# Kernel tuning notes

Measured on AMD Instinct MI355X. Metric: run time of the kernel, lower is better.

Reference implementation:

```python
import jax, jax.numpy as jnp
import numpy as np

NUM_EXPERTS = 8
TOP_K = 2
HIDDEN = 1024
INTER = 3584
TOKENS = 16384


def setup_inputs() -> dict:
    key = jax.random.key(0)
    k0, k1, k2, k3, k4 = jax.random.split(key, 5)
    s = 0.02
    return {
        "hidden_states": jax.random.normal(k0, (TOKENS, HIDDEN), dtype=jnp.float32),
        "gate_w": jax.random.normal(k1, (NUM_EXPERTS, HIDDEN), dtype=jnp.float32) * s,
        "w1": jax.random.normal(k2, (NUM_EXPERTS, INTER, HIDDEN), dtype=jnp.float32) * s,
        "w3": jax.random.normal(k3, (NUM_EXPERTS, INTER, HIDDEN), dtype=jnp.float32) * s,
        "w2": jax.random.normal(k4, (NUM_EXPERTS, HIDDEN, INTER), dtype=jnp.float32) * s,
    }


def reference(hidden_states, gate_w, w1, w3, w2):
    # Router: logits -> softmax -> top-k -> renormalize (Mixtral gating)
    router_logits = jnp.einsum("th,eh->te", hidden_states, gate_w)  # [T, E]
    probs = jax.nn.softmax(router_logits, axis=-1)
    topk_w, topk_idx = jax.lax.top_k(probs, TOP_K)                  # [T, K]
    topk_w = topk_w / jnp.sum(topk_w, axis=-1, keepdims=True)
    # Dense combine weights: [T, E], zero for unselected experts
    combine = jnp.sum(
        jax.nn.one_hot(topk_idx, NUM_EXPERTS, dtype=hidden_states.dtype)
        * topk_w[..., None],
        axis=1,
    )
    out = jnp.zeros_like(hidden_states)
    for e in range(NUM_EXPERTS):  # small fixed expert loop
        h = jnp.einsum("th,ih->ti", hidden_states, w1[e])   # gate proj
        u = jnp.einsum("th,ih->ti", hidden_states, w3[e])   # up proj
        act = jax.nn.silu(h) * u                             # SwiGLU
        y = jnp.einsum("ti,hi->th", act, w2[e])              # down proj
        out = out + combine[:, e:e + 1] * y
    return out
```

## Files before the change

### kernel.cpp

```cpp
#include <hip/hip_runtime.h>
#include <hip/hip_bf16.h>

#define T_TOKENS 16384
#define HID 1024
#define NEXP 8
#define INTER 3584
#define PAIRS (2*T_TOKENS)
#define PAD_MAX (PAIRS + NEXP*128)

using f32x4    = __attribute__((ext_vector_type(4))) float;
using bfrag    = __attribute__((ext_vector_type(8))) short;
using float4_t = __attribute__((ext_vector_type(4))) float;
using ushort8_t = __attribute__((ext_vector_type(8))) unsigned short;

__device__ inline unsigned short f2bf(float f){
    unsigned u = __float_as_uint(f);
    u += 0x7FFFu + ((u >> 16) & 1u);
    return (unsigned short)(u >> 16);
}

__device__ inline void gload16(const unsigned short* g, unsigned short* l){
    __builtin_amdgcn_global_load_lds(
        (const __attribute__((address_space(1))) void*)g,
        (__attribute__((address_space(3))) void*)l, 16, 0, 0);
}

#define BAR_VM8() asm volatile("s_waitcnt vmcnt(8)\n\ts_barrier" ::: "memory")
#define BAR_VM0() asm volatile("s_waitcnt vmcnt(0)\n\ts_barrier" ::: "memory")
#define BAR_PLAIN() asm volatile("s_barrier" ::: "memory")

__device__ inline int xcd_swz(int flat, int nwg){
    int q = nwg >> 3, r = nwg & 7;
    int xcd = flat & 7, idx = flat >> 3;
    return (xcd < r ? xcd*(q+1) : r*(q+1) + (xcd - r)*q) + idx;
}

__device__ inline void st_decode(int sw, int nM, int nP, int STM,
                                 int& mt, int& p){
    int stSize = STM * nP;
    int st = sw / stSize;
    int rem = sw - st * stSize;
    int base = st * STM;
    int stM = (base + STM <= nM) ? STM : (nM - base);
    p  = rem / stM;
    mt = base + (rem - p * stM);
}

__global__ __launch_bounds__(256) void conv3_kernel(
    const float* __restrict__ w1, const float* __restrict__ w3,
    const float* __restrict__ w2,
    unsigned short* __restrict__ w1b, unsigned short* __restrict__ w3b,
    unsigned short* __restrict__ w2b)
{
    const int n = NEXP * INTER * HID;
    const float* in = (blockIdx.y == 0) ? w1 : (blockIdx.y == 1) ? w3 : w2;
    unsigned short* out = (blockIdx.y == 0) ? w1b : (blockIdx.y == 1) ? w3b : w2b;
    int i0 = (blockIdx.x * 256 + threadIdx.x) * 8;
    int stride = gridDim.x * 256 * 8;
    for (int i = i0; i < n; i += stride){
        float4_t a = *reinterpret_cast<const float4_t*>(in + i);
        float4_t b = *reinterpret_cast<const float4_t*>(in + i + 4);
        ushort8_t o;
        o[0]=f2bf(a.x); o[1]=f2bf(a.y); o[2]=f2bf(a.z); o[3]=f2bf(a.w);
        o[4]=f2bf(b.x); o[5]=f2bf(b.y); o[6]=f2bf(b.z); o[7]=f2bf(b.w);
        *reinterpret_cast<ushort8_t*>(out + i) = o;
    }
}

__global__ __launch_bounds__(256) void router_kernel(
    const float* __restrict__ x, const float* __restrict__ gw,
    int* __restrict__ topk_idx, float* __restrict__ topk_w,
    unsigned short* __restrict__ xb)
{
    int wave = threadIdx.x >> 6;
    int lane = threadIdx.x & 63;
    int t = blockIdx.x * 4 + wave;

    float acc[NEXP];
#pragma unroll
    for (int e = 0; e < NEXP; ++e) acc[e] = 0.f;

    const float* xr = x + (size_t)t * HID;
    for (int hb = 0; hb < HID; hb += 64){
        float xv = xr[hb + lane];
#pragma unroll
        for (int e = 0; e < NEXP; ++e)
            acc[e] += xv * gw[e * HID + hb + lane];
    }

    unsigned short* xbr = xb + (size_t)t * HID;
#pragma unroll
    for (int r = 0; r < 2; ++r){
        int c = (lane + r*64) * 8;
        float4_t va = *reinterpret_cast<const float4_t*>(xr + c);
        float4_t vb = *reinterpret_cast<const float4_t*>(xr + c + 4);
        ushort8_t o;
        o[0]=f2bf(va.x); o[1]=f2bf(va.y); o[2]=f2bf(va.z); o[3]=f2bf(va.w);
        o[4]=f2bf(vb.x); o[5]=f2bf(vb.y); o[6]=f2bf(vb.z); o[7]=f2bf(vb.w);
        *reinterpret_cast<ushort8_t*>(xbr + c) = o;
    }

#pragma unroll
    for (int e = 0; e < NEXP; ++e){
#pragma unroll
        for (int s = 32; s > 0; s >>= 1)
            acc[e] += __shfl_xor(acc[e], s, 64);
    }
    if (lane == 0){
        int e0 = 0; float m0 = acc[0];
#pragma unroll
        for (int e = 1; e < NEXP; ++e) if (acc[e] > m0){ m0 = acc[e]; e0 = e; }
        int e1 = -1; float m1 = -1e30f;
#pragma unroll
        for (int e = 0; e < NEXP; ++e) if (e != e0 && acc[e] > m1){ m1 = acc[e]; e1 = e; }
        float p1 = __expf(m1 - m0);
        float inv = 1.f / (1.f + p1);
        topk_idx[2*t]   = e0;
        topk_idx[2*t+1] = e1;
        topk_w[2*t]   = inv;
        topk_w[2*t+1] = p1 * inv;
    }
}

__global__ __launch_bounds__(256) void hist_kernel(
    const int* __restrict__ topk_idx, int* __restrict__ counts)
{
    __shared__ int h[NEXP];
    if (threadIdx.x < NEXP) h[threadIdx.x] = 0;
    __syncthreads();
    int i0 = blockIdx.x * 256 + threadIdx.x;
    for (int i = i0; i < PAIRS; i += gridDim.x * 256)
        atomicAdd(&h[topk_idx[i]], 1);
    __syncthreads();
    if (threadIdx.x < NEXP) atomicAdd(&counts[threadIdx.x], h[threadIdx.x]);
}

__global__ void scan_kernel(const int* __restrict__ counts, int* __restrict__ offp)
{
    if (threadIdx.x == 0 && blockIdx.x == 0){
        int s = 0;
        for (int e = 0; e < NEXP; ++e){
            offp[e] = s;
            s += (counts[e] + 127) & ~127;
        }
        offp[NEXP] = s;
    }
}

__global__ __launch_bounds__(128) void padfill_kernel(
    const int* __restrict__ counts, const int* __restrict__ offp,
    int* __restrict__ pair_token, float* __restrict__ pair_w)
{
    int e = blockIdx.x;
    int base = offp[e];
    int aligned = offp[e+1] - base;
    for (int s = counts[e] + threadIdx.x; s < aligned; s += 128){
        pair_token[base + s] = (base + s) & (T_TOKENS - 1);
        pair_w[base + s] = 0.f;
    }
}

__global__ __launch_bounds__(256) void scatter_kernel(
    const int* __restrict__ topk_idx, const float* __restrict__ topk_w,
    const int* __restrict__ offp, int* __restrict__ cursors,
    int* __restrict__ pair_token, float* __restrict__ pair_w)
{
    __shared__ int hist[NEXP], base[NEXP], lcur[NEXP];
    int tid = threadIdx.x;
    if (tid < NEXP){ hist[tid] = 0; lcur[tid] = 0; }
    __syncthreads();

    int t = blockIdx.x * 256 + tid;
    int e0 = topk_idx[2*t], e1 = topk_idx[2*t + 1];
    atomicAdd(&hist[e0], 1);
    atomicAdd(&hist[e1], 1);
    __syncthreads();

    if (tid < NEXP) base[tid] = atomicAdd(&cursors[tid], hist[tid]);
    __syncthreads();

    int r0 = atomicAdd(&lcur[e0], 1);
    int r1 = atomicAdd(&lcur[e1], 1);
    int p0 = offp[e0] + base[e0] + r0;
    int p1 = offp[e1] + base[e1] + r1;
    pair_token[p0] = t;  pair_w[p0] = topk_w[2*t];
    pair_token[p1] = t;  pair_w[p1] = topk_w[2*t + 1];
}

__global__ __launch_bounds__(256) void gemm_act_kernel(
    const unsigned short* __restrict__ xb,
    const unsigned short* __restrict__ w1b,
    const unsigned short* __restrict__ w3b,
    const int* __restrict__ offp,
    const int* __restrict__ pair_token, const float* __restrict__ pair_w,
    unsigned short* __restrict__ act, int r0)
{
    int nP = gridDim.x, nM = gridDim.y;
    int sw = xcd_swz(blockIdx.y * nP + blockIdx.x, nP * nM);
    int mt, p;
    st_decode(sw, nM, nP, 8, mt, p);
    int by = mt, bx = p;

    int R = r0 + by * 128;
    if (R >= offp[NEXP]) return;
    int e = 0;
    while (offp[e+1] <= R) ++e;
    int icol0 = bx * 64;

    __shared__ alignas(16) unsigned short As0[128*64], As1[128*64];
    __shared__ alignas(16) unsigned short B10[64*64],  B11[64*64];
    __shared__ alignas(16) unsigned short B30[64*64],  B31[64*64];
    __shared__ int   toks[128];
    __shared__ float pws[128];

    int tid = threadIdx.x;
    if (tid < 128){
        toks[tid] = pair_token[R + tid];
        pws[tid]  = pair_w[R + tid];
    }
    __syncthreads();

    int w = tid >> 6, lane = tid & 63;
    int wm = w >> 1, wn = w & 1;
    int lr = lane >> 3;
    int l15 = lane & 15;
    int swz8 = ((lane & 7) ^ lr) * 8;

    size_t asrc[4];
#pragma unroll
    for (int i = 0; i < 4; ++i)
        asrc[i] = (size_t)toks[w*32 + i*8 + lr] * HID + swz8;

    const unsigned short* w1e = w1b + (size_t)e * INTER * HID;
    const unsigned short* w3e = w3b + (size_t)e * INTER * HID;
    size_t bsrc[2];
#pragma unroll
    for (int i = 0; i < 2; ++i)
        bsrc[i] = (size_t)(icol0 + w*16 + i*8 + lr) * HID + swz8;

    int ccol[2];
#pragma unroll
    for (int kk = 0; kk < 2; ++kk)
        ccol[kk] = (((kk*4 + (lane >> 4)) ^ (lane & 7)) * 8);

    f32x4 acc_h[4][2], acc_u[4][2];
#pragma unroll
    for (int m = 0; m < 4; ++m)
#pragma unroll
        for (int n = 0; n < 2; ++n){
            acc_h[m][n] = (f32x4){0.f,0.f,0.f,0.f};
            acc_u[m][n] = (f32x4){0.f,0.f,0.f,0.f};
        }

    auto stageT = [&](unsigned short* As, unsigned short* B1s, unsigned short* B3s, int t){
        int k0 = t * 64;
#pragma unroll
        for (int i = 0; i < 4; ++i) gload16(xb  + asrc[i] + k0, As  + (w*32 + i*8)*64);
#pragma unroll
        for (int i = 0; i < 2; ++i) gload16(w1e + bsrc[i] + k0, B1s + (w*16 + i*8)*64);
#pragma unroll
        for (int i = 0; i < 2; ++i) gload16(w3e + bsrc[i] + k0, B3s + (w*16 + i*8)*64);
    };

    auto computeT = [&](const unsigned short* As, const unsigned short* B1s, const unsigned short* B3s){
        __builtin_amdgcn_s_setprio(1);
#pragma unroll
        for (int kk = 0; kk < 2; ++kk){
            int cc = ccol[kk];
            bfrag a[4];
#pragma unroll
            for (int m = 0; m < 4; ++m)
                a[m] = *reinterpret_cast<const bfrag*>(&As[(wm*64 + m*16 + l15)*64 + cc]);
#pragma unroll
            for (int n = 0; n < 2; ++n){
                bfrag b1 = *reinterpret_cast<const bfrag*>(&B1s[(wn*32 + n*16 + l15)*64 + cc]);
                bfrag b3 = *reinterpret_cast<const bfrag*>(&B3s[(wn*32 + n*16 + l15)*64 + cc]);
#pragma unroll
                for (int m = 0; m < 4; ++m){
                    acc_h[m][n] = __builtin_amdgcn_mfma_f32_16x16x32_bf16(a[m], b1, acc_h[m][n], 0, 0, 0);
                    acc_u[m][n] = __builtin_amdgcn_mfma_f32_16x16x32_bf16(a[m], b3, acc_u[m][n], 0, 0, 0);
                }
            }
        }
        __builtin_amdgcn_s_setprio(0);
    };

    const int NT = HID / 64;
    stageT(As0, B10, B30, 0);
    stageT(As1, B11, B31, 1);
#pragma unroll 1
    for (int t = 0; t < NT - 2; t += 2){
        BAR_VM8();
        computeT(As0, B10, B30);
        BAR_PLAIN();
        stageT(As0, B10, B30, t + 2);
        BAR_VM8();
        computeT(As1, B11, B31);
        BAR_PLAIN();
        stageT(As1, B11, B31, t + 3);
    }
    BAR_VM8();
    computeT(As0, B10, B30);
    BAR_VM0();
    computeT(As1, B11, B31);

    size_t arow0 = (size_t)(by * 128) * INTER;
#pragma unroll
    for (int m = 0; m < 4; ++m){
#pragma unroll
        for (int n = 0; n < 2; ++n){
#pragma unroll
            for (int j = 0; j < 4; ++j){
                int rl = wm*64 + m*16 + (lane >> 4)*4 + j;
                float h = acc_h[m][n][j];
                float u = acc_u[m][n][j];
                float v = pws[rl] * h * u / (1.f + __expf(-h));
                int ic = icol0 + wn*32 + n*16 + l15;
                act[arow0 + (size_t)rl * INTER + ic] = f2bf(v);
            }
        }
    }
}

__global__ __launch_bounds__(256) void gemm2_kernel(
    const unsigned short* __restrict__ act,
    const unsigned short* __restrict__ w2b,
    const int* __restrict__ offp,
    const int* __restrict__ pair_token,
    float* __restrict__ out, int r0)
{
    int nP = gridDim.x, nM = gridDim.y;
    int sw = xcd_swz(blockIdx.y * nP + blockIdx.x, nP * nM);
    int mt, p;
    st_decode(sw, nM, nP, 4, mt, p);
    int by = mt, bx = p;

    int R = r0 + by * 128;
    if (R >= offp[NEXP]) return;
    int e = 0;
    while (offp[e+1] <= R) ++e;
    int h0 = bx * 128;

    __shared__ alignas(16) unsigned short As0[128*64], As1[128*64];
    __shared__ alignas(16) unsigned short Bs0[128*64], Bs1[128*64];
    __shared__ int toks[128];

    int tid = threadIdx.x;
    if (tid < 128) toks[tid] = pair_token[R + tid];
    __syncthreads();

    int w = tid >> 6, lane = tid & 63;
    int wm = w >> 1, wn = w & 1;
    int lr = lane >> 3;
    int l15 = lane & 15;
    int swz8 = ((lane & 7) ^ lr) * 8;

    const unsigned short* w2e = w2b + (size_t)e * HID * INTER;
    size_t arow0 = (size_t)(by * 128) * INTER;

    size_t asrc[4], bsrc[4];
#pragma unroll
    for (int i = 0; i < 4; ++i){
        asrc[i] = arow0 + (size_t)(w*32 + i*8 + lr) * INTER + swz8;
        bsrc[i] = (size_t)(h0 + w*32 + i*8 + lr) * INTER + swz8;
    }

    int ccol[2];
#pragma unroll
    for (int kk = 0; kk < 2; ++kk)
        ccol[kk] = (((kk*4 + (lane >> 4)) ^ (lane & 7)) * 8);

    f32x4 acc[4][4];
#pragma unroll
    for (int m = 0; m < 4; ++m)
#pragma unroll
        for (int n = 0; n < 4; ++n)
            acc[m][n] = (f32x4){0.f,0.f,0.f,0.f};

    auto stageT = [&](unsigned short* As, unsigned short* Bs, int t){
        int kc = t * 64;
#pragma unroll
        for (int i = 0; i < 4; ++i) gload16(act + asrc[i] + kc, As + (w*32 + i*8)*64);
#pragma unroll
        for (int i = 0; i < 4; ++i) gload16(w2e + bsrc[i] + kc, Bs + (w*32 + i*8)*64);
    };

    auto computeT = [&](const unsigned short* As, const unsigned short* Bs){
        __builtin_amdgcn_s_setprio(1);
#pragma unroll
        for (int kk = 0; kk < 2; ++kk){
            int cc = ccol[kk];
            bfrag a[4];
#pragma unroll
            for (int m = 0; m < 4; ++m)
                a[m] = *reinterpret_cast<const bfrag*>(&As[(wm*64 + m*16 + l15)*64 + cc]);
#pragma unroll
            for (int n = 0; n < 4; ++n){
                bfrag b = *reinterpret_cast<const bfrag*>(&Bs[(wn*64 + n*16 + l15)*64 + cc]);
#pragma unroll
                for (int m = 0; m < 4; ++m)
                    acc[m][n] = __builtin_amdgcn_mfma_f32_16x16x32_bf16(a[m], b, acc[m][n], 0, 0, 0);
            }
        }
        __builtin_amdgcn_s_setprio(0);
    };

    const int NT = INTER / 64;
    stageT(As0, Bs0, 0);
    stageT(As1, Bs1, 1);
#pragma unroll 1
    for (int t = 0; t < NT - 2; t += 2){
        BAR_VM8();
        computeT(As0, Bs0);
        BAR_PLAIN();
        stageT(As0, Bs0, t + 2);
        BAR_VM8();
        computeT(As1, Bs1);
        BAR_PLAIN();
        stageT(As1, Bs1, t + 3);
    }
    BAR_VM8();
    computeT(As0, Bs0);
    BAR_VM0();
    computeT(As1, Bs1);

#pragma unroll
    for (int m = 0; m < 4; ++m){
#pragma unroll
        for (int n = 0; n < 4; ++n){
#pragma unroll
            for (int j = 0; j < 4; ++j){
                int rl = wm*64 + m*16 + (lane >> 4)*4 + j;
                int hc = h0 + wn*64 + n*16 + l15;
                atomicAdd(&out[(size_t)toks[rl] * HID + hc], acc[m][n][j]);
            }
        }
    }
}

extern "C" void kernel_launch(void* const* d_in, const int* in_sizes, int n_in,
                              void* d_out, int out_size, void* d_ws, size_t ws_size,
                              hipStream_t stream)
{
    const float* x  = (const float*)d_in[0];
    const float* gw = (const float*)d_in[1];
    const float* w1 = (const float*)d_in[2];
    const float* w3 = (const float*)d_in[3];
    const float* w2 = (const float*)d_in[4];
    float* out = (float*)d_out;

    char* ws = (char*)d_ws;
    size_t off = 0;
    auto bump = [&](size_t bytes) -> void* {
        void* p = ws + off;
        off = (off + bytes + 255) & ~(size_t)255;
        return p;
    };
    int*   counts     = (int*)bump(32);
    int*   cursors    = (int*)bump(32);
    int*   offp       = (int*)bump(64);
    int*   topk_idx   = (int*)bump((size_t)PAIRS * 4);
    float* topk_w     = (float*)bump((size_t)PAIRS * 4);
    int*   pair_token = (int*)bump((size_t)PAD_MAX * 4);
    float* pair_w     = (float*)bump((size_t)PAD_MAX * 4);
    unsigned short* xb  = (unsigned short*)bump((size_t)T_TOKENS * HID * 2);
    unsigned short* w1b = (unsigned short*)bump((size_t)NEXP * INTER * HID * 2);
    unsigned short* w3b = (unsigned short*)bump((size_t)NEXP * INTER * HID * 2);
    unsigned short* w2b = (unsigned short*)bump((size_t)NEXP * HID * INTER * 2);
    unsigned short* act = (unsigned short*)(ws + off);

    size_t rem = (ws_size > off) ? (ws_size - off) : 0;
    int RC = (int)(rem / ((size_t)INTER * 2));
    RC &= ~127;
    if (RC > PAD_MAX) RC = PAD_MAX;
    if (RC < 128) RC = 128;
    int nchunks = (PAD_MAX + RC - 1) / RC;

    hipMemsetAsync(d_out, 0, (size_t)T_TOKENS * HID * 4, stream);
    hipMemsetAsync(ws, 0, 1024, stream);

    conv3_kernel<<<dim3(768, 3), 256, 0, stream>>>(w1, w3, w2, w1b, w3b, w2b);

    router_kernel<<<T_TOKENS/4, 256, 0, stream>>>(x, gw, topk_idx, topk_w, xb);
    hist_kernel<<<64, 256, 0, stream>>>(topk_idx, counts);
    scan_kernel<<<1, 64, 0, stream>>>(counts, offp);
    padfill_kernel<<<NEXP, 128, 0, stream>>>(counts, offp, pair_token, pair_w);
    scatter_kernel<<<T_TOKENS/256, 256, 0, stream>>>(topk_idx, topk_w, offp, cursors,
                                                     pair_token, pair_w);

    for (int c = 0; c < nchunks; ++c){
        int r0 = c * RC;
        gemm_act_kernel<<<dim3(INTER/64, RC/128), 256, 0, stream>>>(
            xb, w1b, w3b, offp, pair_token, pair_w, act, r0);
        gemm2_kernel<<<dim3(HID/128, RC/128), 256, 0, stream>>>(
            act, w2b, offp, pair_token, out, r0);
    }
}
```

Before: 1.057 ms.

## Enlarge down-projection GEMM tile to 256x256 with 8-wave ping-pong schedule

The down-projection GEMM now uses 256x256 output tiles with 512 threads (8 waves). Its main loop splits each stage into half-tiles and interleaves LDS fragment reads, global-to-LDS loads and MFMA quadrants under fine-grained barriers. Expert padding is raised to 256 rows so each tile stays within one expert. The larger tile raises arithmetic intensity and cuts redundant loads of activations and weights. In exchange it adds padded rows, uses more registers and LDS per block, and launches fewer blocks.

```diff
diff --git a/kernel.cpp b/kernel.cpp
--- a/kernel.cpp
+++ b/kernel.cpp
@@ -6,7 +6,7 @@
 #define NEXP 8
 #define INTER 3584
 #define PAIRS (2*T_TOKENS)
-#define PAD_MAX (PAIRS + NEXP*128)
+#define PAD_MAX (PAIRS + NEXP*256)
 
 using f32x4    = __attribute__((ext_vector_type(4))) float;
 using bfrag    = __attribute__((ext_vector_type(8))) short;
@@ -26,6 +26,7 @@
 }
 
 #define BAR_VM8() asm volatile("s_waitcnt vmcnt(8)\n\ts_barrier" ::: "memory")
+#define BAR_VM4() asm volatile("s_waitcnt vmcnt(4)\n\ts_barrier" ::: "memory")
 #define BAR_VM0() asm volatile("s_waitcnt vmcnt(0)\n\ts_barrier" ::: "memory")
 #define BAR_PLAIN() asm volatile("s_barrier" ::: "memory")
 
@@ -141,7 +142,7 @@
         int s = 0;
         for (int e = 0; e < NEXP; ++e){
             offp[e] = s;
-            s += (counts[e] + 127) & ~127;
+            s += (counts[e] + 255) & ~255;
         }
         offp[NEXP] = s;
     }
@@ -322,7 +323,7 @@
     }
 }
 
-__global__ __launch_bounds__(256) void gemm2_kernel(
+__global__ __launch_bounds__(512) void gemm2_kernel(
     const unsigned short* __restrict__ act,
     const unsigned short* __restrict__ w2b,
     const int* __restrict__ offp,
@@ -332,106 +333,158 @@
     int nP = gridDim.x, nM = gridDim.y;
     int sw = xcd_swz(blockIdx.y * nP + blockIdx.x, nP * nM);
     int mt, p;
-    st_decode(sw, nM, nP, 4, mt, p);
+    st_decode(sw, nM, nP, 2, mt, p);
     int by = mt, bx = p;
 
-    int R = r0 + by * 128;
+    int R = r0 + by * 256;
     if (R >= offp[NEXP]) return;
     int e = 0;
     while (offp[e+1] <= R) ++e;
-    int h0 = bx * 128;
-
-    __shared__ alignas(16) unsigned short As0[128*64], As1[128*64];
-    __shared__ alignas(16) unsigned short Bs0[128*64], Bs1[128*64];
-    __shared__ int toks[128];
+    int h0 = bx * 256;
+
+    __shared__ alignas(16) unsigned short As0s[256*64], Bs0s[256*64];
+    __shared__ alignas(16) unsigned short As1s[256*64], Bs1s[256*64];
+    __shared__ int toks[256];
 
     int tid = threadIdx.x;
-    if (tid < 128) toks[tid] = pair_token[R + tid];
+    if (tid < 256) toks[tid] = pair_token[R + tid];
     __syncthreads();
 
     int w = tid >> 6, lane = tid & 63;
-    int wm = w >> 1, wn = w & 1;
-    int lr = lane >> 3;
+    int wm = w >> 2, wn = w & 3;
     int l15 = lane & 15;
-    int swz8 = ((lane & 7) ^ lr) * 8;
+    int sr = tid >> 3;
+    int swzc8 = ((tid & 7) ^ (sr & 7)) * 8;
 
     const unsigned short* w2e = w2b + (size_t)e * HID * INTER;
-    size_t arow0 = (size_t)(by * 128) * INTER;
-
-    size_t asrc[4], bsrc[4];
-#pragma unroll
-    for (int i = 0; i < 4; ++i){
-        asrc[i] = arow0 + (size_t)(w*32 + i*8 + lr) * INTER + swz8;
-        bsrc[i] = (size_t)(h0 + w*32 + i*8 + lr) * INTER + swz8;
-    }
+    size_t arow0 = (size_t)(by * 256) * INTER;
+
+    size_t aoff0 = arow0 + (size_t)sr * INTER + swzc8;
+    size_t aoff1 = aoff0 + (size_t)64 * INTER;
+    size_t boff0 = (size_t)(h0 + sr) * INTER + swzc8;
+    size_t boff1 = boff0 + (size_t)64 * INTER;
 
     int ccol[2];
 #pragma unroll
     for (int kk = 0; kk < 2; ++kk)
         ccol[kk] = (((kk*4 + (lane >> 4)) ^ (lane & 7)) * 8);
 
-    f32x4 acc[4][4];
-#pragma unroll
-    for (int m = 0; m < 4; ++m)
+    f32x4 acc[8][4];
+#pragma unroll
+    for (int m = 0; m < 8; ++m)
 #pragma unroll
         for (int n = 0; n < 4; ++n)
             acc[m][n] = (f32x4){0.f,0.f,0.f,0.f};
 
-    auto stageT = [&](unsigned short* As, unsigned short* Bs, int t){
+    bfrag asub[4][2];
+    bfrag bsub[2][2];
+
+    auto stA = [&](unsigned short* As, int h, int t){
         int kc = t * 64;
-#pragma unroll
-        for (int i = 0; i < 4; ++i) gload16(act + asrc[i] + kc, As + (w*32 + i*8)*64);
-#pragma unroll
-        for (int i = 0; i < 4; ++i) gload16(w2e + bsrc[i] + kc, Bs + (w*32 + i*8)*64);
-    };
-
-    auto computeT = [&](const unsigned short* As, const unsigned short* Bs){
+        gload16(act + aoff0 + (size_t)h*(128*INTER) + kc, As + h*8192 + tid*8);
+        gload16(act + aoff1 + (size_t)h*(128*INTER) + kc, As + h*8192 + 4096 + tid*8);
+    };
+    auto stB = [&](unsigned short* Bs, int h, int t){
+        int kc = t * 64;
+        gload16(w2e + boff0 + (size_t)h*(128*INTER) + kc, Bs + h*8192 + tid*8);
+        gload16(w2e + boff1 + (size_t)h*(128*INTER) + kc, Bs + h*8192 + 4096 + tid*8);
+    };
+
+    auto dsA = [&](const unsigned short* As, int Mh){
+#pragma unroll
+        for (int mfl = 0; mfl < 4; ++mfl)
+#pragma unroll
+            for (int kk = 0; kk < 2; ++kk)
+                asub[mfl][kk] = *reinterpret_cast<const bfrag*>(
+                    &As[(Mh*128 + wm*64 + mfl*16 + l15)*64 + ccol[kk]]);
+    };
+    auto dsB = [&](const unsigned short* Bs, int Nh){
+#pragma unroll
+        for (int nf = 0; nf < 2; ++nf)
+#pragma unroll
+            for (int kk = 0; kk < 2; ++kk)
+                bsub[nf][kk] = *reinterpret_cast<const bfrag*>(
+                    &Bs[(Nh*128 + wn*32 + nf*16 + l15)*64 + ccol[kk]]);
+    };
+    auto mma = [&](int Mh, int Nh){
         __builtin_amdgcn_s_setprio(1);
 #pragma unroll
-        for (int kk = 0; kk < 2; ++kk){
-            int cc = ccol[kk];
-            bfrag a[4];
-#pragma unroll
-            for (int m = 0; m < 4; ++m)
-                a[m] = *reinterpret_cast<const bfrag*>(&As[(wm*64 + m*16 + l15)*64 + cc]);
-#pragma unroll
-            for (int n = 0; n < 4; ++n){
-                bfrag b = *reinterpret_cast<const bfrag*>(&Bs[(wn*64 + n*16 + l15)*64 + cc]);
-#pragma unroll
-                for (int m = 0; m < 4; ++m)
-                    acc[m][n] = __builtin_amdgcn_mfma_f32_16x16x32_bf16(a[m], b, acc[m][n], 0, 0, 0);
-            }
-        }
+        for (int kk = 0; kk < 2; ++kk)
+#pragma unroll
+            for (int nf = 0; nf < 2; ++nf)
+#pragma unroll
+                for (int mfl = 0; mfl < 4; ++mfl)
+                    acc[Mh*4+mfl][Nh*2+nf] = __builtin_amdgcn_mfma_f32_16x16x32_bf16(
+                        asub[mfl][kk], bsub[nf][kk], acc[Mh*4+mfl][Nh*2+nf], 0, 0, 0);
         __builtin_amdgcn_s_setprio(0);
     };
 
     const int NT = INTER / 64;
-    stageT(As0, Bs0, 0);
-    stageT(As1, Bs1, 1);
+
+    stB(Bs0s, 0, 0);
+    stA(As0s, 1, 0);
+    stA(As0s, 0, 0);
+    stB(Bs0s, 1, 0);
+    stB(Bs1s, 0, 1);
+    stA(As1s, 1, 1);
+    BAR_VM4();
+
 #pragma unroll 1
-    for (int t = 0; t < NT - 2; t += 2){
-        BAR_VM8();
-        computeT(As0, Bs0);
-        BAR_PLAIN();
-        stageT(As0, Bs0, t + 2);
-        BAR_VM8();
-        computeT(As1, Bs1);
-        BAR_PLAIN();
-        stageT(As1, Bs1, t + 3);
-    }
-    BAR_VM8();
-    computeT(As0, Bs0);
-    BAR_VM0();
-    computeT(As1, Bs1);
-
-#pragma unroll
-    for (int m = 0; m < 4; ++m){
+    for (int i = 0; i < NT/2 - 1; ++i){
+        int t1 = 2*i + 1, t2 = 2*i + 2, t3 = 2*i + 3;
+        dsA(As0s, 0); dsB(Bs0s, 0);
+        stA(As1s, 0, t1);
+        BAR_PLAIN(); mma(0, 0); BAR_PLAIN();
+        dsA(As0s, 1);
+        stB(Bs1s, 1, t1);
+        BAR_PLAIN(); mma(1, 0); BAR_PLAIN();
+        dsB(Bs0s, 1);
+        stB(Bs0s, 0, t2);
+        BAR_PLAIN(); mma(1, 1); BAR_PLAIN();
+        dsA(As0s, 0);
+        stA(As0s, 1, t2);
+        BAR_VM4(); mma(0, 1); BAR_PLAIN();
+        dsA(As1s, 0); dsB(Bs1s, 0);
+        stA(As0s, 0, t2);
+        BAR_PLAIN(); mma(0, 0); BAR_PLAIN();
+        dsA(As1s, 1);
+        stB(Bs0s, 1, t2);
+        BAR_PLAIN(); mma(1, 0); BAR_PLAIN();
+        dsB(Bs1s, 1);
+        stB(Bs1s, 0, t3);
+        BAR_PLAIN(); mma(1, 1); BAR_PLAIN();
+        dsA(As1s, 0);
+        stA(As1s, 1, t3);
+        BAR_VM4(); mma(0, 1); BAR_PLAIN();
+    }
+
+    dsA(As0s, 0); dsB(Bs0s, 0);
+    stA(As1s, 0, NT-1);
+    BAR_PLAIN(); mma(0, 0); BAR_PLAIN();
+    dsA(As0s, 1);
+    stB(Bs1s, 1, NT-1);
+    BAR_PLAIN(); mma(1, 0); BAR_PLAIN();
+    dsB(Bs0s, 1);
+    BAR_PLAIN(); mma(1, 1); BAR_PLAIN();
+    dsA(As0s, 0);
+    BAR_VM0(); mma(0, 1); BAR_PLAIN();
+    dsA(As1s, 0); dsB(Bs1s, 0);
+    BAR_PLAIN(); mma(0, 0); BAR_PLAIN();
+    dsA(As1s, 1);
+    BAR_PLAIN(); mma(1, 0); BAR_PLAIN();
+    dsB(Bs1s, 1);
+    BAR_PLAIN(); mma(1, 1); BAR_PLAIN();
+    dsA(As1s, 0);
+    BAR_PLAIN(); mma(0, 1); BAR_PLAIN();
+
+#pragma unroll
+    for (int m = 0; m < 8; ++m){
 #pragma unroll
         for (int n = 0; n < 4; ++n){
 #pragma unroll
             for (int j = 0; j < 4; ++j){
-                int rl = wm*64 + m*16 + (lane >> 4)*4 + j;
-                int hc = h0 + wn*64 + n*16 + l15;
+                int rl = (m >> 2)*128 + wm*64 + (m & 3)*16 + (lane >> 4)*4 + j;
+                int hc = h0 + (n >> 1)*128 + wn*32 + (n & 1)*16 + l15;
                 atomicAdd(&out[(size_t)toks[rl] * HID + hc], acc[m][n][j]);
             }
         }
@@ -471,9 +524,9 @@
 
     size_t rem = (ws_size > off) ? (ws_size - off) : 0;
     int RC = (int)(rem / ((size_t)INTER * 2));
-    RC &= ~127;
+    RC &= ~255;
     if (RC > PAD_MAX) RC = PAD_MAX;
-    if (RC < 128) RC = 128;
+    if (RC < 256) RC = 256;
     int nchunks = (PAD_MAX + RC - 1) / RC;
 
     hipMemsetAsync(d_out, 0, (size_t)T_TOKENS * HID * 4, stream);
@@ -492,7 +545,7 @@
         int r0 = c * RC;
         gemm_act_kernel<<<dim3(INTER/64, RC/128), 256, 0, stream>>>(
             xb, w1b, w3b, offp, pair_token, pair_w, act, r0);
-        gemm2_kernel<<<dim3(HID/128, RC/128), 256, 0, stream>>>(
+        gemm2_kernel<<<dim3(HID/256, RC/256), 512, 0, stream>>>(
             act, w2b, offp, pair_token, out, r0);
     }
 }
```

After: 1.168 ms. 10.5% more time.
